# Kernel optimization log

Measured on AMD Instinct MI355X. Metric: run time of the kernel, lower is better.

Reference implementation:

```python
import jax, jax.numpy as jnp
import numpy as np

WS = 32          # window_size -> N = WS*WS = 1024
DIM = 1024
HEADS = 16
BATCH = 16


def _local_mask():
    # token i maps to grid cell (i//WS, i%WS); attend iff within 3x3 neighborhood
    idx = jnp.arange(WS * WS)
    r, c = idx // WS, idx % WS
    return (jnp.abs(r[:, None] - r[None, :]) <= 1) & (jnp.abs(c[:, None] - c[None, :]) <= 1)


def setup_inputs() -> dict:
    key = jax.random.key(0)
    k1, k2, k3 = jax.random.split(key, 3)
    N = WS * WS
    x = jax.random.normal(k1, (BATCH, N, DIM), dtype=jnp.float32)
    w_qkv = jax.random.normal(k2, (3 * DIM, DIM), dtype=jnp.float32) * 0.02
    w_proj = jax.random.normal(k3, (DIM, DIM), dtype=jnp.float32) * 0.02
    b_proj = jnp.zeros((DIM,), dtype=jnp.float32)
    return {"x": x, "w_qkv": w_qkv, "w_proj": w_proj, "b_proj": b_proj}


def reference(x, w_qkv, w_proj, b_proj):
    B, N, C = x.shape
    H = HEADS
    D = C // H
    scale = D ** (-0.5)
    # qkv projection: torch Linear is x @ W^T
    qkv = (x @ w_qkv.T).reshape(B, N, 3, H, D).transpose(2, 0, 3, 1, 4)  # (3,B,H,N,D)
    q, k, v = qkv[0], qkv[1], qkv[2]
    attn = jnp.einsum('bhnd,bhmd->bhnm', q, k) * scale  # (B,H,N,N)
    mask = _local_mask()  # (N,N) bool
    attn = jnp.where(mask[None, None], attn, -jnp.inf)
    attn = jax.nn.softmax(attn, axis=-1)
    out = jnp.einsum('bhnm,bhmd->bhnd', attn, v)          # (B,H,N,D)
    out = out.transpose(0, 2, 1, 3).reshape(B, N, C)      # (B,N,C)
    return out @ w_proj.T + b_proj
```

## Files before the change

kernel.cpp:

```cpp
#include <hip/hip_runtime.h>
#include <hip/hip_bf16.h>
#include <stdint.h>


typedef __bf16 bf16;
typedef __bf16 bf16x4_t __attribute__((ext_vector_type(4)));
typedef __bf16 bf16x8_t __attribute__((ext_vector_type(8)));
typedef float f32x4_t __attribute__((ext_vector_type(4)));

static __device__ __forceinline__ void gload_lds16(const void* g, void* l) {
  __builtin_amdgcn_global_load_lds((__attribute__((address_space(1))) void*)g,
                                   (__attribute__((address_space(3))) void*)l,
                                   16, 0, 0);
}

static __device__ __forceinline__ void block_barrier() {
  asm volatile("" ::: "memory");
  __builtin_amdgcn_s_barrier();
  asm volatile("" ::: "memory");
}

__global__ void cvt_all(const float* __restrict__ x, const float* __restrict__ wq,
                        const float* __restrict__ wp, bf16* __restrict__ xb,
                        bf16* __restrict__ wqb, bf16* __restrict__ wpb) {
  constexpr int NX = 4194304, NWQ = 786432;
  int i = blockIdx.x * blockDim.x + threadIdx.x;
  const float* src; bf16* dst; int off;
  if (i < NX)            { src = x;  dst = xb;  off = i; }
  else if (i < NX + NWQ) { src = wq; dst = wqb; off = i - NX; }
  else                   { src = wp; dst = wpb; off = i - (NX + NWQ); }
  float4 v = reinterpret_cast<const float4*>(src)[off];
  bf16x4_t o;
  o[0] = (bf16)v.x; o[1] = (bf16)v.y; o[2] = (bf16)v.z; o[3] = (bf16)v.w;
  reinterpret_cast<bf16x4_t*>(dst)[off] = o;
}

template<int OUT_BF16>
__global__ __launch_bounds__(512, 2)
void gemm256(const bf16* __restrict__ A, const bf16* __restrict__ Bm,
             void* __restrict__ Cout, const float* __restrict__ bias,
             int M, int N, int K) {
  extern __shared__ __align__(16) bf16 lds[];

  const int tid = threadIdx.x;
  const int w = tid >> 6, lane = tid & 63;
  const int fr = lane & 15, g = lane >> 4;
  const int wr = w >> 2, wc = w & 3;

  const int nwg = gridDim.x * gridDim.y;
  int lid = blockIdx.y * gridDim.x + blockIdx.x;
  lid = (lid & 7) * (nwg >> 3) + (lid >> 3);
  const int bx = lid % gridDim.x, by = lid / gridDim.x;
  const int row0 = by * 256, col0 = bx * 256;

  const bf16* Ag = A + (size_t)row0 * K;
  const bf16* Bg = Bm + (size_t)col0 * K;
  const int rsub = tid >> 3;
  const int csw  = ((tid & 7) * 8) ^ ((rsub & 7) << 3);
  const int nkt  = K >> 6;

  f32x4_t acc[8][4] = {};

  auto stageA = [&](int kt, int slot) {
    const int kb = kt << 6;
    bf16* sl = lds + slot * 32768;
#pragma unroll
    for (int n = 0; n < 4; ++n)
      gload_lds16(Ag + (size_t)(rsub + n * 64) * K + kb + csw,
                  sl + n * 4096 + w * 512);
  };
  auto stageB = [&](int kt, int slot) {
    const int kb = kt << 6;
    bf16* sl = lds + slot * 32768 + 16384;
#pragma unroll
    for (int n = 0; n < 4; ++n)
      gload_lds16(Bg + (size_t)(rsub + n * 64) * K + kb + csw,
                  sl + n * 4096 + w * 512);
  };

  const int axor = (fr & 7) << 4;

  stageB(0, 0); stageA(0, 0);
  stageB(1, 1); stageA(1, 1);
  asm volatile("s_waitcnt vmcnt(8)" ::: "memory");
  block_barrier();

  for (int kt = 0; kt < nkt; ++kt) {
    const char* cA = reinterpret_cast<const char*>(lds + (kt & 1) * 32768);
    const char* cB = cA + 32768;
    const bool pf = (kt + 2 < nkt);

    bf16x8_t a0[4][2], a1[4][2], b0[2][2], b1[2][2];

    auto lda = [&](bf16x8_t (&dst)[4][2], int q) {
#pragma unroll
      for (int i = 0; i < 4; ++i) {
        const int row = wr * 128 + (q * 4 + i) * 16 + fr;
#pragma unroll
        for (int kh = 0; kh < 2; ++kh) {
          const int bo = (row << 7) + (((kh << 6) + (g << 4)) ^ axor);
          dst[i][kh] = *reinterpret_cast<const bf16x8_t*>(cA + bo);
        }
      }
    };
    auto ldb = [&](bf16x8_t (&dst)[2][2], int q) {
#pragma unroll
      for (int j = 0; j < 2; ++j) {
        const int row = wc * 64 + (q * 2 + j) * 16 + fr;
#pragma unroll
        for (int kh = 0; kh < 2; ++kh) {
          const int bo = (row << 7) + (((kh << 6) + (g << 4)) ^ axor);
          dst[j][kh] = *reinterpret_cast<const bf16x8_t*>(cB + bo);
        }
      }
    };
    auto mfma16 = [&](bf16x8_t (&af)[4][2], bf16x8_t (&bf_)[2][2], int mi0, int nj0) {
      __builtin_amdgcn_s_setprio(1);
#pragma unroll
      for (int i = 0; i < 4; ++i)
#pragma unroll
        for (int j = 0; j < 2; ++j)
#pragma unroll
          for (int kh = 0; kh < 2; ++kh)
            acc[mi0 + i][nj0 + j] = __builtin_amdgcn_mfma_f32_16x16x32_bf16(
                af[i][kh], bf_[j][kh], acc[mi0 + i][nj0 + j], 0, 0, 0);
      __builtin_amdgcn_s_setprio(0);
    };

    lda(a0, 0); ldb(b0, 0);
    asm volatile("s_waitcnt lgkmcnt(8)" ::: "memory");
    block_barrier();
    asm volatile("s_waitcnt lgkmcnt(0)" ::: "memory");
    __builtin_amdgcn_sched_barrier(0);
    mfma16(a0, b0, 0, 0);
    block_barrier();

    ldb(b1, 1);
    block_barrier();
    asm volatile("s_waitcnt lgkmcnt(0)" ::: "memory");
    __builtin_amdgcn_sched_barrier(0);
    mfma16(a0, b1, 0, 2);
    block_barrier();

    lda(a1, 1);
    if (pf) stageB(kt + 2, kt & 1);
    block_barrier();
    asm volatile("s_waitcnt lgkmcnt(0)" ::: "memory");
    __builtin_amdgcn_sched_barrier(0);
    mfma16(a1, b1, 4, 2);
    block_barrier();

    if (pf) stageA(kt + 2, kt & 1);
    block_barrier();
    __builtin_amdgcn_sched_barrier(0);
    mfma16(a1, b0, 4, 0);
    if (pf) {
      asm volatile("s_waitcnt vmcnt(8)" ::: "memory");
    } else {
      asm volatile("s_waitcnt vmcnt(0)" ::: "memory");
    }
    block_barrier();
  }

#pragma unroll
  for (int fm = 0; fm < 8; ++fm) {
    const int rbase = row0 + wr * 128 + fm * 16 + g * 4;
#pragma unroll
    for (int fn = 0; fn < 4; ++fn) {
      const int col = col0 + wc * 64 + fn * 16 + fr;
#pragma unroll
      for (int r = 0; r < 4; ++r) {
        const size_t idx = (size_t)(rbase + r) * N + col;
        if constexpr (OUT_BF16) {
          reinterpret_cast<bf16*>(Cout)[idx] = (bf16)acc[fm][fn][r];
        } else {
          reinterpret_cast<float*>(Cout)[idx] = acc[fm][fn][r] + bias[col];
        }
      }
    }
  }
}

__global__ __launch_bounds__(256)
void local_attn(const bf16* __restrict__ qkv, bf16* __restrict__ outp) {
  const int tid  = threadIdx.x;
  const int wave = tid >> 6, lane = tid & 63;
  const int tsub = lane >> 3, ch = lane & 7;
  const int gt = (blockIdx.x * 4 + wave) * 8 + tsub;
  const int i  = gt & 1023;
  const int bh = gt >> 10;
  const int h  = bh & 15, b = bh >> 4;
  const int r  = i >> 5, c = i & 31;

  const bf16* base = qkv + (size_t)(b * 1024) * 3072 + h * 64 + ch * 8;

  bf16x8_t qv = *reinterpret_cast<const bf16x8_t*>(base + (size_t)i * 3072);
  float qf[8];
#pragma unroll
  for (int e = 0; e < 8; ++e) qf[e] = (float)qv[e];

  float s[9];
  bool valid[9];
#pragma unroll
  for (int dr = -1; dr <= 1; ++dr) {
#pragma unroll
    for (int dc = -1; dc <= 1; ++dc) {
      const int idx = (dr + 1) * 3 + (dc + 1);
      const int rr = r + dr, cc = c + dc;
      valid[idx] = (rr >= 0 && rr < 32 && cc >= 0 && cc < 32);
      float sv = -1e30f;
      if (valid[idx]) {
        const int j = rr * 32 + cc;
        bf16x8_t kv = *reinterpret_cast<const bf16x8_t*>(base + (size_t)j * 3072 + 1024);
        float ps = 0.f;
#pragma unroll
        for (int e = 0; e < 8; ++e) ps += qf[e] * (float)kv[e];
        ps += __shfl_xor(ps, 1);
        ps += __shfl_xor(ps, 2);
        ps += __shfl_xor(ps, 4);
        sv = ps * 0.125f;
      }
      s[idx] = sv;
    }
  }

  float mx = s[0];
#pragma unroll
  for (int t = 1; t < 9; ++t) mx = fmaxf(mx, s[t]);

  float p[9], denom = 0.f;
#pragma unroll
  for (int t = 0; t < 9; ++t) {
    p[t] = valid[t] ? __expf(s[t] - mx) : 0.f;
    denom += p[t];
  }

  float o[8] = {};
#pragma unroll
  for (int dr = -1; dr <= 1; ++dr) {
#pragma unroll
    for (int dc = -1; dc <= 1; ++dc) {
      const int idx = (dr + 1) * 3 + (dc + 1);
      if (valid[idx]) {
        const int j = (r + dr) * 32 + (c + dc);
        bf16x8_t vv = *reinterpret_cast<const bf16x8_t*>(base + (size_t)j * 3072 + 2048);
        const float pw = p[idx];
#pragma unroll
        for (int e = 0; e < 8; ++e) o[e] += pw * (float)vv[e];
      }
    }
  }

  const float inv = 1.f / denom;
  bf16x8_t ov;
#pragma unroll
  for (int e = 0; e < 8; ++e) ov[e] = (bf16)(o[e] * inv);
  *reinterpret_cast<bf16x8_t*>(outp + (size_t)(b * 1024 + i) * 1024 + h * 64 + ch * 8) = ov;
}

extern "C" void kernel_launch(void* const* d_in, const int* in_sizes, int n_in,
                              void* d_out, int out_size, void* d_ws, size_t ws_size,
                              hipStream_t stream) {
  const float* x      = (const float*)d_in[0];
  const float* w_qkv  = (const float*)d_in[1];
  const float* w_proj = (const float*)d_in[2];
  const float* b_proj = (const float*)d_in[3];
  float* out = (float*)d_out;

  const size_t nx   = (size_t)16384 * 1024;
  const size_t nwq  = (size_t)3072 * 1024;
  const size_t nwp  = (size_t)1024 * 1024;
  const size_t nqkv = (size_t)16384 * 3072;

  bf16* x_bf  = (bf16*)d_ws;
  bf16* wq_bf = x_bf + nx;
  bf16* wp_bf = wq_bf + nwq;
  bf16* qkv   = wp_bf + nwp;
  bf16* attn  = qkv + nqkv;

  (void)hipFuncSetAttribute((const void*)&gemm256<1>,
                            hipFuncAttributeMaxDynamicSharedMemorySize, 131072);
  (void)hipFuncSetAttribute((const void*)&gemm256<0>,
                            hipFuncAttributeMaxDynamicSharedMemorySize, 131072);

  cvt_all<<<20480, 256, 0, stream>>>(x, w_qkv, w_proj, x_bf, wq_bf, wp_bf);

  gemm256<1><<<dim3(3072 / 256, 16384 / 256), 512, 131072, stream>>>(
      x_bf, wq_bf, qkv, nullptr, 16384, 3072, 1024);

  local_attn<<<8192, 256, 0, stream>>>(qkv, attn);

  gemm256<0><<<dim3(1024 / 256, 16384 / 256), 512, 131072, stream>>>(
      attn, wp_bf, out, b_proj, 16384, 1024, 1024);
}
```

Measured before the change: 217.8 us.

## Split GEMM tile staging into eight quarter-loads interleaved across k-iteration phases

The double-buffered GEMM's global-to-LDS staging is split into eight per-quarter loads (four for A, four for B). Each phase of the four-phase MFMA loop now issues two of them, spreading the prefetch of tiles kt+1 and kt+2 across the iteration instead of clustering it in two bursts. The intent is smoother memory-issue pressure and better overlap of VMEM with MFMA, with a vmcnt(4) wait in place of vmcnt(8). The risk is in the slot reuse: part of tile kt+1 is written into the slot being read only after the earlier barriers, so correctness depends on that barrier ordering.

```diff
diff --git a/kernel.cpp b/kernel.cpp
--- a/kernel.cpp
+++ b/kernel.cpp
@@ -37,10 +37,11 @@
 
 template<int OUT_BF16>
 __global__ __launch_bounds__(512, 2)
-void gemm256(const bf16* __restrict__ A, const bf16* __restrict__ Bm,
-             void* __restrict__ Cout, const float* __restrict__ bias,
-             int M, int N, int K) {
-  extern __shared__ __align__(16) bf16 lds[];
+void gemm8p(const bf16* __restrict__ A, const bf16* __restrict__ Bm,
+            void* __restrict__ Cout, const float* __restrict__ bias,
+            int M, int N, int K) {
+  constexpr int SLOT = 65536;
+  extern __shared__ __align__(16) char lds[];
 
   const int tid = threadIdx.x;
   const int w = tid >> 6, lane = tid & 63;
@@ -55,66 +56,57 @@
 
   const bf16* Ag = A + (size_t)row0 * K;
   const bf16* Bg = Bm + (size_t)col0 * K;
-  const int rsub = tid >> 3;
-  const int csw  = ((tid & 7) * 8) ^ ((rsub & 7) << 3);
+  const int srow = tid >> 3;
+  const int scol = ((tid & 7) ^ (srow & 7)) * 8;
   const int nkt  = K >> 6;
 
   f32x4_t acc[8][4] = {};
 
-  auto stageA = [&](int kt, int slot) {
-    const int kb = kt << 6;
-    bf16* sl = lds + slot * 32768;
-#pragma unroll
-    for (int n = 0; n < 4; ++n)
-      gload_lds16(Ag + (size_t)(rsub + n * 64) * K + kb + csw,
-                  sl + n * 4096 + w * 512);
+  auto stA = [&](int kt, int u) {
+    gload_lds16(Ag + (size_t)(u * 64 + srow) * K + (kt << 6) + scol,
+                lds + (kt & 1) * SLOT + u * 8192 + tid * 16);
   };
-  auto stageB = [&](int kt, int slot) {
-    const int kb = kt << 6;
-    bf16* sl = lds + slot * 32768 + 16384;
-#pragma unroll
-    for (int n = 0; n < 4; ++n)
-      gload_lds16(Bg + (size_t)(rsub + n * 64) * K + kb + csw,
-                  sl + n * 4096 + w * 512);
+  auto stB = [&](int kt, int u) {
+    gload_lds16(Bg + (size_t)(u * 64 + srow) * K + (kt << 6) + scol,
+                lds + (kt & 1) * SLOT + 32768 + u * 8192 + tid * 16);
   };
 
   const int axor = (fr & 7) << 4;
 
-  stageB(0, 0); stageA(0, 0);
-  stageB(1, 1); stageA(1, 1);
-  asm volatile("s_waitcnt vmcnt(8)" ::: "memory");
+  stB(0, 0); stB(0, 1); stA(0, 0); stA(0, 1); stA(0, 2); stA(0, 3);
+  stB(0, 2); stB(0, 3);
+  stB(1, 0); stB(1, 1); stA(1, 0); stA(1, 1);
+  asm volatile("s_waitcnt vmcnt(4)" ::: "memory");
   block_barrier();
 
   for (int kt = 0; kt < nkt; ++kt) {
-    const char* cA = reinterpret_cast<const char*>(lds + (kt & 1) * 32768);
+    const char* cA = lds + (kt & 1) * SLOT;
     const char* cB = cA + 32768;
-    const bool pf = (kt + 2 < nkt);
+    const bool p1 = (kt + 1 < nkt), p2 = (kt + 2 < nkt);
 
     bf16x8_t a0[4][2], a1[4][2], b0[2][2], b1[2][2];
 
-    auto lda = [&](bf16x8_t (&dst)[4][2], int q) {
+    auto lda = [&](bf16x8_t (&d)[4][2], int q) {
 #pragma unroll
       for (int i = 0; i < 4; ++i) {
         const int row = wr * 128 + (q * 4 + i) * 16 + fr;
 #pragma unroll
-        for (int kh = 0; kh < 2; ++kh) {
-          const int bo = (row << 7) + (((kh << 6) + (g << 4)) ^ axor);
-          dst[i][kh] = *reinterpret_cast<const bf16x8_t*>(cA + bo);
-        }
+        for (int kh = 0; kh < 2; ++kh)
+          d[i][kh] = *reinterpret_cast<const bf16x8_t*>(
+              cA + (row << 7) + (((kh << 6) + (g << 4)) ^ axor));
       }
     };
-    auto ldb = [&](bf16x8_t (&dst)[2][2], int q) {
+    auto ldb = [&](bf16x8_t (&d)[2][2], int q) {
 #pragma unroll
       for (int j = 0; j < 2; ++j) {
         const int row = wc * 64 + (q * 2 + j) * 16 + fr;
 #pragma unroll
-        for (int kh = 0; kh < 2; ++kh) {
-          const int bo = (row << 7) + (((kh << 6) + (g << 4)) ^ axor);
-          dst[j][kh] = *reinterpret_cast<const bf16x8_t*>(cB + bo);
-        }
+        for (int kh = 0; kh < 2; ++kh)
+          d[j][kh] = *reinterpret_cast<const bf16x8_t*>(
+              cB + (row << 7) + (((kh << 6) + (g << 4)) ^ axor));
       }
     };
-    auto mfma16 = [&](bf16x8_t (&af)[4][2], bf16x8_t (&bf_)[2][2], int mi0, int nj0) {
+    auto mf = [&](bf16x8_t (&a)[4][2], bf16x8_t (&b)[2][2], int mi, int nj) {
       __builtin_amdgcn_s_setprio(1);
 #pragma unroll
       for (int i = 0; i < 4; ++i)
@@ -122,43 +114,42 @@
         for (int j = 0; j < 2; ++j)
 #pragma unroll
           for (int kh = 0; kh < 2; ++kh)
-            acc[mi0 + i][nj0 + j] = __builtin_amdgcn_mfma_f32_16x16x32_bf16(
-                af[i][kh], bf_[j][kh], acc[mi0 + i][nj0 + j], 0, 0, 0);
+            acc[mi + i][nj + j] = __builtin_amdgcn_mfma_f32_16x16x32_bf16(
+                a[i][kh], b[j][kh], acc[mi + i][nj + j], 0, 0, 0);
       __builtin_amdgcn_s_setprio(0);
     };
 
     lda(a0, 0); ldb(b0, 0);
+    if (p1) { stA(kt + 1, 2); stA(kt + 1, 3); }
     asm volatile("s_waitcnt lgkmcnt(8)" ::: "memory");
     block_barrier();
     asm volatile("s_waitcnt lgkmcnt(0)" ::: "memory");
     __builtin_amdgcn_sched_barrier(0);
-    mfma16(a0, b0, 0, 0);
+    mf(a0, b0, 0, 0);
     block_barrier();
 
     ldb(b1, 1);
+    if (p1) { stB(kt + 1, 2); stB(kt + 1, 3); }
     block_barrier();
     asm volatile("s_waitcnt lgkmcnt(0)" ::: "memory");
     __builtin_amdgcn_sched_barrier(0);
-    mfma16(a0, b1, 0, 2);
+    mf(a0, b1, 0, 2);
     block_barrier();
 
     lda(a1, 1);
-    if (pf) stageB(kt + 2, kt & 1);
+    if (p2) { stB(kt + 2, 0); stB(kt + 2, 1); }
     block_barrier();
     asm volatile("s_waitcnt lgkmcnt(0)" ::: "memory");
     __builtin_amdgcn_sched_barrier(0);
-    mfma16(a1, b1, 4, 2);
-    block_barrier();
-
-    if (pf) stageA(kt + 2, kt & 1);
-    block_barrier();
-    __builtin_amdgcn_sched_barrier(0);
-    mfma16(a1, b0, 4, 0);
-    if (pf) {
-      asm volatile("s_waitcnt vmcnt(8)" ::: "memory");
-    } else {
-      asm volatile("s_waitcnt vmcnt(0)" ::: "memory");
-    }
+    mf(a1, b1, 4, 2);
+    block_barrier();
+
+    if (p2) { stA(kt + 2, 0); stA(kt + 2, 1); }
+    block_barrier();
+    __builtin_amdgcn_sched_barrier(0);
+    mf(a1, b0, 4, 0);
+    if (p2) asm volatile("s_waitcnt vmcnt(4)" ::: "memory");
+    else    asm volatile("s_waitcnt vmcnt(0)" ::: "memory");
     block_barrier();
   }
 
@@ -278,18 +269,18 @@
   bf16* qkv   = wp_bf + nwp;
   bf16* attn  = qkv + nqkv;
 
-  (void)hipFuncSetAttribute((const void*)&gemm256<1>,
+  (void)hipFuncSetAttribute((const void*)&gemm8p<1>,
                             hipFuncAttributeMaxDynamicSharedMemorySize, 131072);
-  (void)hipFuncSetAttribute((const void*)&gemm256<0>,
+  (void)hipFuncSetAttribute((const void*)&gemm8p<0>,
                             hipFuncAttributeMaxDynamicSharedMemorySize, 131072);
 
   cvt_all<<<20480, 256, 0, stream>>>(x, w_qkv, w_proj, x_bf, wq_bf, wp_bf);
 
-  gemm256<1><<<dim3(3072 / 256, 16384 / 256), 512, 131072, stream>>>(
+  gemm8p<1><<<dim3(3072 / 256, 16384 / 256), 512, 131072, stream>>>(
       x_bf, wq_bf, qkv, nullptr, 16384, 3072, 1024);
 
   local_attn<<<8192, 256, 0, stream>>>(qkv, attn);
 
-  gemm256<0><<<dim3(1024 / 256, 16384 / 256), 512, 131072, stream>>>(
+  gemm8p<0><<<dim3(1024 / 256, 16384 / 256), 512, 131072, stream>>>(
       attn, wp_bf, out, b_proj, 16384, 1024, 1024);
 }
```

Measured after the change: 217.1 us. About the same (-0.3%).
